# Optimization experiments

Measured on AMD Instinct MI355X. Metric: run time of the kernel, lower is better.

Reference implementation:

```python
import jax, jax.numpy as jnp
import numpy as np


def setup_inputs() -> dict:
    key = jax.random.key(0)
    k1, k2, k3, k4 = jax.random.split(key, 4)
    H, B, S = 1024, 32, 4096
    hidden = jax.random.normal(k1, (1, B, H), dtype=jnp.float32)
    encoder_outputs = jax.random.normal(k2, (S, B, H), dtype=jnp.float32)
    attn_W = jax.random.normal(k3, (H, H), dtype=jnp.float32) * (1.0 / np.sqrt(H))
    attn_b = jax.random.normal(k4, (H,), dtype=jnp.float32) * 0.01
    return {"hidden": hidden, "encoder_outputs": encoder_outputs,
            "attn_W": attn_W, "attn_b": attn_b}


def reference(hidden, encoder_outputs, attn_W, attn_b):
    # method == 'general':
    #   energy[b, i] = hidden[0, b] . (attn_W @ encoder_outputs[i, b] + attn_b)
    # Linear: enc @ W.T + b, applied over [S, B, H]
    proj = jnp.einsum('sbh,gh->sbg', encoder_outputs, attn_W) + attn_b  # [S, B, H]
    energies = jnp.einsum('bh,sbh->bs', hidden[0], proj)               # [B, S]
    # F.softmax on 2D defaults to last dim (seq dim), then unsqueeze(1)
    normalized = jax.nn.softmax(energies, axis=-1)[:, None, :]         # [B, 1, S]
    return normalized
```

## Files before the change

kernel.cpp:

```cpp
#include <hip/hip_runtime.h>
#include <math.h>

constexpr int H = 1024;
constexpr int B = 32;
constexpr int S = 4096;

__global__ __launch_bounds__(256) void compute_v_kernel(
    const float* __restrict__ hidden, const float* __restrict__ W,
    float* __restrict__ v)
{
    const int b  = blockIdx.x >> 4;
    const int hc = blockIdx.x & 15;
    const int hq = threadIdx.x & 15;
    const int gg = threadIdx.x >> 4;
    const int hquad = hc * 16 + hq;
    const float* __restrict__ hb = hidden + b * H;
    const float4* __restrict__ W4 = (const float4*)W;

    float4 aE = {0,0,0,0}, aO = {0,0,0,0};
    const int g0 = gg * 64;
    #pragma unroll 4
    for (int g = g0; g < g0 + 64; g += 2) {
        float  h0 = hb[g], h1 = hb[g + 1];
        float4 w0 = W4[(size_t)(g + 0) * 256 + hquad];
        float4 w1 = W4[(size_t)(g + 1) * 256 + hquad];
        aE.x = fmaf(h0, w0.x, aE.x); aE.y = fmaf(h0, w0.y, aE.y);
        aE.z = fmaf(h0, w0.z, aE.z); aE.w = fmaf(h0, w0.w, aE.w);
        aO.x = fmaf(h1, w1.x, aO.x); aO.y = fmaf(h1, w1.y, aO.y);
        aO.z = fmaf(h1, w1.z, aO.z); aO.w = fmaf(h1, w1.w, aO.w);
    }
    float4 acc = {aE.x + aO.x, aE.y + aO.y, aE.z + aO.z, aE.w + aO.w};

    __shared__ float4 part[16][16];
    part[gg][hq] = acc;
    __syncthreads();
    if (threadIdx.x < 64) {
        const int q  = threadIdx.x & 15;
        const int kk = threadIdx.x >> 4;
        float4 s = part[kk * 4 + 0][q];
        #pragma unroll
        for (int j = 1; j < 4; ++j) {
            float4 p = part[kk * 4 + j][q];
            s.x += p.x; s.y += p.y; s.z += p.z; s.w += p.w;
        }
        part[kk * 4][q] = s;
    }
    __syncthreads();
    if (threadIdx.x < 16) {
        const int q = threadIdx.x;
        float4 s = part[0][q];
        #pragma unroll
        for (int j = 1; j < 4; ++j) {
            float4 p = part[j * 4][q];
            s.x += p.x; s.y += p.y; s.z += p.z; s.w += p.w;
        }
        ((float4*)(v + b * H))[hquad] = s;
    }
}

#define LOAD8(pfx, pA, pB)                                                   \
    pfx##a0 = (pA)[lane];        pfx##a1 = (pA)[64 + lane];                  \
    pfx##a2 = (pA)[128 + lane];  pfx##a3 = (pA)[192 + lane];                 \
    pfx##b0 = (pB)[lane];        pfx##b1 = (pB)[64 + lane];                  \
    pfx##b2 = (pB)[128 + lane];  pfx##b3 = (pB)[192 + lane];

#define COMPUTE_STORE(pfx, kk)                                               \
    {                                                                        \
        float pa0 = pfx##a0.x * wa0.x, pa1 = pfx##a1.x * wa1.x;              \
        float pb0 = pfx##b0.x * wb0.x, pb1 = pfx##b1.x * wb1.x;              \
        pa0 = fmaf(pfx##a0.y, wa0.y, pa0); pa1 = fmaf(pfx##a1.y, wa1.y, pa1);\
        pb0 = fmaf(pfx##b0.y, wb0.y, pb0); pb1 = fmaf(pfx##b1.y, wb1.y, pb1);\
        pa0 = fmaf(pfx##a0.z, wa0.z, pa0); pa1 = fmaf(pfx##a1.z, wa1.z, pa1);\
        pb0 = fmaf(pfx##b0.z, wb0.z, pb0); pb1 = fmaf(pfx##b1.z, wb1.z, pb1);\
        pa0 = fmaf(pfx##a0.w, wa0.w, pa0); pa1 = fmaf(pfx##a1.w, wa1.w, pa1);\
        pb0 = fmaf(pfx##b0.w, wb0.w, pb0); pb1 = fmaf(pfx##b1.w, wb1.w, pb1);\
        pa0 = fmaf(pfx##a2.x, wa2.x, pa0); pa1 = fmaf(pfx##a3.x, wa3.x, pa1);\
        pb0 = fmaf(pfx##b2.x, wb2.x, pb0); pb1 = fmaf(pfx##b3.x, wb3.x, pb1);\
        pa0 = fmaf(pfx##a2.y, wa2.y, pa0); pa1 = fmaf(pfx##a3.y, wa3.y, pa1);\
        pb0 = fmaf(pfx##b2.y, wb2.y, pb0); pb1 = fmaf(pfx##b3.y, wb3.y, pb1);\
        pa0 = fmaf(pfx##a2.z, wa2.z, pa0); pa1 = fmaf(pfx##a3.z, wa3.z, pa1);\
        pb0 = fmaf(pfx##b2.z, wb2.z, pb0); pb1 = fmaf(pfx##b3.z, wb3.z, pb1);\
        pa0 = fmaf(pfx##a2.w, wa2.w, pa0); pa1 = fmaf(pfx##a3.w, wa3.w, pa1);\
        pb0 = fmaf(pfx##b2.w, wb2.w, pb0); pb1 = fmaf(pfx##b3.w, wb3.w, pb1);\
        float pa = pa0 + pa1;                                                \
        float pb = pb0 + pb1;                                                \
        _Pragma("unroll")                                                    \
        for (int off = 32; off > 0; off >>= 1) {                             \
            pa += __shfl_xor(pa, off, 64);                                   \
            pb += __shfl_xor(pb, off, 64);                                   \
        }                                                                    \
        if (lane == 0) {                                                     \
            energies[(size_t)b0 * S + s_base + (kk)] = pa;                   \
            energies[(size_t)b1 * S + s_base + (kk)] = pb;                   \
        }                                                                    \
    }

__global__ __launch_bounds__(1024) void energies_kernel(
    const float* __restrict__ enc, const float* __restrict__ v,
    float* __restrict__ energies)
{
    const int w    = threadIdx.x >> 6;
    const int lane = threadIdx.x & 63;
    const int b0 = w, b1 = w + 16;
    const size_t base   = (size_t)blockIdx.x * 512;
    const int    s_base = blockIdx.x * 16;

    const float4* __restrict__ v4 = (const float4*)v;
    const float4 wa0 = v4[b0 * 256 + lane],       wa1 = v4[b0 * 256 + 64 + lane],
                 wa2 = v4[b0 * 256 + 128 + lane], wa3 = v4[b0 * 256 + 192 + lane];
    const float4 wb0 = v4[b1 * 256 + lane],       wb1 = v4[b1 * 256 + 64 + lane],
                 wb2 = v4[b1 * 256 + 128 + lane], wb3 = v4[b1 * 256 + 192 + lane];

    const float4* __restrict__ rbase = (const float4*)enc + (base + (size_t)w) * 256;

    float4 xa0, xa1, xa2, xa3, xb0, xb1, xb2, xb3;
    float4 ya0, ya1, ya2, ya3, yb0, yb1, yb2, yb3;

    { const float4* pA = rbase; const float4* pB = rbase + 4096;
      LOAD8(x, pA, pB) }

    #pragma unroll
    for (int k = 0; k < 16; k += 2) {
        { const float4* pA = rbase + (size_t)(k + 1) * 8192;
          const float4* pB = pA + 4096;
          LOAD8(y, pA, pB) }
        COMPUTE_STORE(x, k)
        if (k + 2 < 16) {
            const float4* pA = rbase + (size_t)(k + 2) * 8192;
            const float4* pB = pA + 4096;
            LOAD8(x, pA, pB)
        }
        COMPUTE_STORE(y, k + 1)
    }
}

__global__ __launch_bounds__(1024) void softmax_kernel(float* __restrict__ out)
{
    const int b = blockIdx.x;
    float4* __restrict__ row4 = (float4*)(out + (size_t)b * S);
    const int w = threadIdx.x >> 6;
    const int lane = threadIdx.x & 63;
    __shared__ float redm[16];
    __shared__ float reds[16];

    float4 x = row4[threadIdx.x];
    float m = fmaxf(fmaxf(x.x, x.y), fmaxf(x.z, x.w));
    #pragma unroll
    for (int off = 32; off > 0; off >>= 1)
        m = fmaxf(m, __shfl_xor(m, off, 64));
    if (lane == 0) redm[w] = m;
    __syncthreads();
    float M = redm[0];
    #pragma unroll
    for (int i = 1; i < 16; ++i) M = fmaxf(M, redm[i]);

    float4 e;
    e.x = __expf(x.x - M); e.y = __expf(x.y - M);
    e.z = __expf(x.z - M); e.w = __expf(x.w - M);
    float s = (e.x + e.y) + (e.z + e.w);
    #pragma unroll
    for (int off = 32; off > 0; off >>= 1)
        s += __shfl_xor(s, off, 64);
    if (lane == 0) reds[w] = s;
    __syncthreads();
    float T = reds[0];
    #pragma unroll
    for (int i = 1; i < 16; ++i) T += reds[i];
    const float inv = 1.0f / T;
    e.x *= inv; e.y *= inv; e.z *= inv; e.w *= inv;
    row4[threadIdx.x] = e;
}

extern "C" void kernel_launch(void* const* d_in, const int* in_sizes, int n_in,
                              void* d_out, int out_size, void* d_ws, size_t ws_size,
                              hipStream_t stream) {
    const float* hidden = (const float*)d_in[0];
    const float* enc    = (const float*)d_in[1];
    const float* W      = (const float*)d_in[2];
    float* out = (float*)d_out;
    float* v   = (float*)d_ws;

    compute_v_kernel<<<dim3(B * 16), dim3(256), 0, stream>>>(hidden, W, v);
    energies_kernel<<<dim3(256), dim3(1024), 0, stream>>>(enc, v, out);
    softmax_kernel<<<dim3(B), dim3(1024), 0, stream>>>(out);
}
```

Baseline: 112.0 us.

## Restructure v computation to reuse W across batch, nontemporal encoder loads

New measurement: 106.9 us. 1.05x faster.

```diff
diff --git a/kernel.cpp b/kernel.cpp
--- a/kernel.cpp
+++ b/kernel.cpp
@@ -5,64 +5,59 @@
 constexpr int B = 32;
 constexpr int S = 4096;
 
+typedef float f4 __attribute__((ext_vector_type(4)));
+#define NTL(p) __builtin_nontemporal_load(p)
+
 __global__ __launch_bounds__(256) void compute_v_kernel(
     const float* __restrict__ hidden, const float* __restrict__ W,
     float* __restrict__ v)
 {
-    const int b  = blockIdx.x >> 4;
-    const int hc = blockIdx.x & 15;
-    const int hq = threadIdx.x & 15;
-    const int gg = threadIdx.x >> 4;
-    const int hquad = hc * 16 + hq;
-    const float* __restrict__ hb = hidden + b * H;
-    const float4* __restrict__ W4 = (const float4*)W;
+    extern __shared__ float smem[];
+    const int tid = threadIdx.x;
+    const int b   = tid & 31;
+    const int gs  = tid >> 5;
+    const int hq  = blockIdx.x;
 
-    float4 aE = {0,0,0,0}, aO = {0,0,0,0};
-    const int g0 = gg * 64;
+    for (int i = tid; i < B * H; i += 256) {
+        const int bb = i >> 10, g = i & 1023;
+        smem[(bb << 10) | (g ^ bb)] = hidden[i];
+    }
+    __syncthreads();
+
+    const f4* __restrict__ Wq = (const f4*)W;
+    const float* __restrict__ hrow = smem + (b << 10);
+    f4 acc = {0.f, 0.f, 0.f, 0.f};
+    const int g0 = gs * 128;
     #pragma unroll 4
-    for (int g = g0; g < g0 + 64; g += 2) {
-        float  h0 = hb[g], h1 = hb[g + 1];
-        float4 w0 = W4[(size_t)(g + 0) * 256 + hquad];
-        float4 w1 = W4[(size_t)(g + 1) * 256 + hquad];
-        aE.x = fmaf(h0, w0.x, aE.x); aE.y = fmaf(h0, w0.y, aE.y);
-        aE.z = fmaf(h0, w0.z, aE.z); aE.w = fmaf(h0, w0.w, aE.w);
-        aO.x = fmaf(h1, w1.x, aO.x); aO.y = fmaf(h1, w1.y, aO.y);
-        aO.z = fmaf(h1, w1.z, aO.z); aO.w = fmaf(h1, w1.w, aO.w);
+    for (int j = 0; j < 128; ++j) {
+        const int g = g0 + j;
+        const float hv = hrow[g ^ b];
+        const f4 wv = Wq[(size_t)g * 256 + hq];
+        acc.x = fmaf(hv, wv.x, acc.x);
+        acc.y = fmaf(hv, wv.y, acc.y);
+        acc.z = fmaf(hv, wv.z, acc.z);
+        acc.w = fmaf(hv, wv.w, acc.w);
     }
-    float4 acc = {aE.x + aO.x, aE.y + aO.y, aE.z + aO.z, aE.w + aO.w};
-
-    __shared__ float4 part[16][16];
-    part[gg][hq] = acc;
     __syncthreads();
-    if (threadIdx.x < 64) {
-        const int q  = threadIdx.x & 15;
-        const int kk = threadIdx.x >> 4;
-        float4 s = part[kk * 4 + 0][q];
+    f4* part = (f4*)smem;
+    part[(gs << 5) | b] = acc;
+    __syncthreads();
+    if (tid < 32) {
+        f4 s = part[tid];
         #pragma unroll
-        for (int j = 1; j < 4; ++j) {
-            float4 p = part[kk * 4 + j][q];
+        for (int k = 1; k < 8; ++k) {
+            const f4 p = part[(k << 5) | tid];
             s.x += p.x; s.y += p.y; s.z += p.z; s.w += p.w;
         }
-        part[kk * 4][q] = s;
-    }
-    __syncthreads();
-    if (threadIdx.x < 16) {
-        const int q = threadIdx.x;
-        float4 s = part[0][q];
-        #pragma unroll
-        for (int j = 1; j < 4; ++j) {
-            float4 p = part[j * 4][q];
-            s.x += p.x; s.y += p.y; s.z += p.z; s.w += p.w;
-        }
-        ((float4*)(v + b * H))[hquad] = s;
+        ((f4*)v)[tid * 256 + hq] = s;
     }
 }
 
 #define LOAD8(pfx, pA, pB)                                                   \
-    pfx##a0 = (pA)[lane];        pfx##a1 = (pA)[64 + lane];                  \
-    pfx##a2 = (pA)[128 + lane];  pfx##a3 = (pA)[192 + lane];                 \
-    pfx##b0 = (pB)[lane];        pfx##b1 = (pB)[64 + lane];                  \
-    pfx##b2 = (pB)[128 + lane];  pfx##b3 = (pB)[192 + lane];
+    pfx##a0 = NTL((pA) + lane);        pfx##a1 = NTL((pA) + 64 + lane);      \
+    pfx##a2 = NTL((pA) + 128 + lane);  pfx##a3 = NTL((pA) + 192 + lane);     \
+    pfx##b0 = NTL((pB) + lane);        pfx##b1 = NTL((pB) + 64 + lane);      \
+    pfx##b2 = NTL((pB) + 128 + lane);  pfx##b3 = NTL((pB) + 192 + lane);
 
 #define COMPUTE_STORE(pfx, kk)                                               \
     {                                                                        \
@@ -101,33 +96,33 @@
 {
     const int w    = threadIdx.x >> 6;
     const int lane = threadIdx.x & 63;
-    const int b0 = w, b1 = w + 16;
+    const int b0 = 2 * w, b1 = 2 * w + 1;
     const size_t base   = (size_t)blockIdx.x * 512;
     const int    s_base = blockIdx.x * 16;
 
-    const float4* __restrict__ v4 = (const float4*)v;
-    const float4 wa0 = v4[b0 * 256 + lane],       wa1 = v4[b0 * 256 + 64 + lane],
-                 wa2 = v4[b0 * 256 + 128 + lane], wa3 = v4[b0 * 256 + 192 + lane];
-    const float4 wb0 = v4[b1 * 256 + lane],       wb1 = v4[b1 * 256 + 64 + lane],
-                 wb2 = v4[b1 * 256 + 128 + lane], wb3 = v4[b1 * 256 + 192 + lane];
+    const f4* __restrict__ v4 = (const f4*)v;
+    const f4 wa0 = v4[b0 * 256 + lane],       wa1 = v4[b0 * 256 + 64 + lane],
+             wa2 = v4[b0 * 256 + 128 + lane], wa3 = v4[b0 * 256 + 192 + lane];
+    const f4 wb0 = v4[b1 * 256 + lane],       wb1 = v4[b1 * 256 + 64 + lane],
+             wb2 = v4[b1 * 256 + 128 + lane], wb3 = v4[b1 * 256 + 192 + lane];
 
-    const float4* __restrict__ rbase = (const float4*)enc + (base + (size_t)w) * 256;
+    const f4* __restrict__ rbase = (const f4*)enc + (base + 2u * w) * 256;
 
-    float4 xa0, xa1, xa2, xa3, xb0, xb1, xb2, xb3;
-    float4 ya0, ya1, ya2, ya3, yb0, yb1, yb2, yb3;
+    f4 xa0, xa1, xa2, xa3, xb0, xb1, xb2, xb3;
+    f4 ya0, ya1, ya2, ya3, yb0, yb1, yb2, yb3;
 
-    { const float4* pA = rbase; const float4* pB = rbase + 4096;
+    { const f4* pA = rbase; const f4* pB = rbase + 256;
       LOAD8(x, pA, pB) }
 
     #pragma unroll
     for (int k = 0; k < 16; k += 2) {
-        { const float4* pA = rbase + (size_t)(k + 1) * 8192;
-          const float4* pB = pA + 4096;
+        { const f4* pA = rbase + (size_t)(k + 1) * 8192;
+          const f4* pB = pA + 256;
           LOAD8(y, pA, pB) }
         COMPUTE_STORE(x, k)
         if (k + 2 < 16) {
-            const float4* pA = rbase + (size_t)(k + 2) * 8192;
-            const float4* pB = pA + 4096;
+            const f4* pA = rbase + (size_t)(k + 2) * 8192;
+            const f4* pB = pA + 256;
             LOAD8(x, pA, pB)
         }
         COMPUTE_STORE(y, k + 1)
@@ -180,7 +175,7 @@
     float* out = (float*)d_out;
     float* v   = (float*)d_ws;
 
-    compute_v_kernel<<<dim3(B * 16), dim3(256), 0, stream>>>(hidden, W, v);
+    compute_v_kernel<<<dim3(256), dim3(256), 32 * 1024 * 4, stream>>>(hidden, W, v);
     energies_kernel<<<dim3(256), dim3(1024), 0, stream>>>(enc, v, out);
     softmax_kernel<<<dim3(B), dim3(1024), 0, stream>>>(out);
 }
```
